# Kernel optimization log

Measured on AMD Instinct MI355X. Metric: run time of the kernel, lower is better.

Reference implementation:

```python
import jax, jax.numpy as jnp
import numpy as np
from jax import lax

B, C, H, W = 32, 512, 14, 14
NA = 9
N = H * W * NA  # 1764 anchors per image
IOU_THR = 0.3
SCORE_THR = 0.5
TOPK = 50


def setup_inputs() -> dict:
    key = jax.random.key(0)
    ks = jax.random.split(key, 8)
    def w(k, shape):
        return jax.random.normal(k, shape, jnp.float32) * 0.01  # nn.init.normal_(std=0.01)
    inp = {"features": jax.random.normal(ks[0], (B, C, H, W), jnp.float32)}
    # bbox head: 512->256 (GN32) ->128 (GN16) ->128 (GN16) -> 4*NA (1x1)
    inp["b1w"] = w(ks[1], (256, 512, 3, 3)); inp["b1b"] = jnp.zeros(256)
    inp["bg1w"] = jnp.ones(256); inp["bg1b"] = jnp.zeros(256)
    inp["b2w"] = w(ks[2], (128, 256, 3, 3)); inp["b2b"] = jnp.zeros(128)
    inp["bg2w"] = jnp.ones(128); inp["bg2b"] = jnp.zeros(128)
    inp["b3w"] = w(ks[3], (128, 128, 3, 3)); inp["b3b"] = jnp.zeros(128)
    inp["bg3w"] = jnp.ones(128); inp["bg3b"] = jnp.zeros(128)
    inp["b4w"] = w(ks[4], (4 * NA, 128, 1, 1)); inp["b4b"] = jnp.zeros(4 * NA)
    # classification head: 512->256 (GN32) ->128 (GN16) -> NA (1x1)
    inp["c1w"] = w(ks[5], (256, 512, 3, 3)); inp["c1b"] = jnp.zeros(256)
    inp["cg1w"] = jnp.ones(256); inp["cg1b"] = jnp.zeros(256)
    inp["c2w"] = w(ks[6], (128, 256, 3, 3)); inp["c2b"] = jnp.zeros(128)
    inp["cg2w"] = jnp.ones(128); inp["cg2b"] = jnp.zeros(128)
    inp["c3w"] = w(ks[7], (NA, 128, 1, 1)); inp["c3b"] = jnp.zeros(NA)
    return inp


def conv(x, w, b):
    k = w.shape[-1]
    pad = ((k // 2, k // 2), (k // 2, k // 2))
    y = lax.conv_general_dilated(x, w, (1, 1), pad, dimension_numbers=("NCHW", "OIHW", "NCHW"))
    return y + b[None, :, None, None]


def group_norm(x, w, b, groups, eps=1e-5):
    Bn, Cn, Hn, Wn = x.shape
    xg = x.reshape(Bn, groups, Cn // groups, Hn, Wn)
    mu = xg.mean(axis=(2, 3, 4), keepdims=True)
    var = xg.var(axis=(2, 3, 4), keepdims=True)
    xg = (xg - mu) * lax.rsqrt(var + eps)
    return xg.reshape(Bn, Cn, Hn, Wn) * w[None, :, None, None] + b[None, :, None, None]


def gelu(x):
    return jax.nn.gelu(x, approximate=False)  # torch nn.GELU default (erf)


def nms_single(boxes, scores):
    # boxes [N,4], scores [N]; greedy NMS, fixed-shape padded output [TOPK,5]
    valid = scores > SCORE_THR
    boxes = jnp.clip(boxes, 0.0, 1.0)
    order = jnp.argsort(-jnp.where(valid, scores, -jnp.inf))  # desc, invalid last
    b = boxes[order]; s = scores[order]; v = valid[order]
    x1 = jnp.maximum(b[:, None, 0], b[None, :, 0])
    y1 = jnp.maximum(b[:, None, 1], b[None, :, 1])
    x2 = jnp.minimum(b[:, None, 2], b[None, :, 2])
    y2 = jnp.minimum(b[:, None, 3], b[None, :, 3])
    inter = jnp.clip(x2 - x1, 0.0) * jnp.clip(y2 - y1, 0.0)
    area = (b[:, 2] - b[:, 0]) * (b[:, 3] - b[:, 1])
    iou = inter / (area[:, None] + area[None, :] - inter)
    # torch keeps when iou < thr; NaN compares False -> suppressed. Replicate exactly:
    suppress = jnp.logical_not(iou < IOU_THR)  # [N,N] bool
    idxs = jnp.arange(N)
    def body(suppressed, xs):
        row, i, vi = xs
        keep_i = vi & jnp.logical_not(suppressed[i])
        return suppressed | (keep_i & row & (idxs > i)), keep_i
    _, keep = lax.scan(body, jnp.zeros(N, bool), (suppress, idxs, v))
    kept_scores = jnp.where(keep, s, -1.0)
    topv, topi = lax.top_k(kept_scores, TOPK)  # first <=50 kept in score order
    out_boxes = jnp.where(topv[:, None] > 0.0, b[topi], 0.0)
    return jnp.concatenate([out_boxes, topv[:, None]], axis=-1)  # [TOPK, 5]; score=-1 marks pad


def _forward(features, b1w, b1b, bg1w, bg1b, b2w, b2b, bg2w, bg2b, b3w, b3b, bg3w, bg3b, b4w, b4b, c1w, c1b, cg1w, cg1b, c2w, c2b, cg2w, cg2b, c3w, c3b):
    bs = features.shape[0]
    h = group_norm(gelu(conv(features, b1w, b1b)), bg1w, bg1b, 32)
    h = group_norm(gelu(conv(h, b2w, b2b)), bg2w, bg2b, 16)
    h = group_norm(gelu(conv(h, b3w, b3b)), bg3w, bg3b, 16)
    bbox = conv(h, b4w, b4b).transpose(0, 2, 3, 1).reshape(bs, -1, 4)  # [B,N,4]
    h = group_norm(gelu(conv(features, c1w, c1b)), cg1w, cg1b, 32)
    h = group_norm(gelu(conv(h, c2w, c2b)), cg2w, cg2b, 16)
    conf = jax.nn.sigmoid(conv(h, c3w, c3b).transpose(0, 2, 3, 1).reshape(bs, -1))  # [B,N]
    return jax.vmap(nms_single)(bbox, conf)  # [B,TOPK,5]


def reference(features, b1w, b1b, bg1w, bg1b, b2w, b2b, bg2w, bg2b, b3w, b3b, bg3w, bg3b, b4w, b4b, c1w, c1b, cg1w, cg1b, c2w, c2b, cg2w, cg2b, c3w, c3b):
    return _forward(features, b1w, b1b, bg1w, bg1b, b2w, b2b, bg2w, bg2b, b3w, b3b, bg3w, bg3b, b4w, b4b, c1w, c1b, cg1w, cg1b, c2w, c2b, cg2w, cg2b, c3w, c3b)
```

## Files before the change

kernel.cpp:

```cpp
#include <hip/hip_runtime.h>
#include <hip/hip_bf16.h>
#include <math.h>

#define CHUNK 16
#define NN 1764
#define SORTN 2048

typedef float v2f __attribute__((ext_vector_type(2)));

template<int Co, int Ci>
__device__ inline void seg_pack_pk(const float* __restrict__ src, float* __restrict__ dst, int i) {
  int co = i / (Ci * 9); int rem = i - co * (Ci * 9); int ci = rem / 9; int k = rem - ci * 9;
  int p = (co >> 5) * 16 + (co & 15);
  int h = (co & 31) >> 4;
  dst[((size_t)ci * (Co >> 1) + p) * 20 + 2 * k + h] = src[i];
}
template<int Co, int CiK>
__device__ inline void seg_tr(const float* __restrict__ src, float* __restrict__ dst, int i) {
  int co = i / CiK; int cik = i - co * CiK;
  dst[cik * Co + co] = src[i];
}

__device__ inline void seg_wino_u(const float* __restrict__ src, float* __restrict__ dst, int i) {
  int ci = i >> 8;
  int co = i & 255;
  const float* g = src + ((size_t)co * 512 + ci) * 9;
  float g00=g[0],g01=g[1],g02=g[2],g10=g[3],g11=g[4],g12=g[5],g20=g[6],g21=g[7],g22=g[8];
  float a[4][3];
  a[0][0]=g00; a[0][1]=g01; a[0][2]=g02;
  a[1][0]=0.5f*(g00+g10+g20); a[1][1]=0.5f*(g01+g11+g21); a[1][2]=0.5f*(g02+g12+g22);
  a[2][0]=0.5f*(g00-g10+g20); a[2][1]=0.5f*(g01-g11+g21); a[2][2]=0.5f*(g02-g12+g22);
  a[3][0]=g20; a[3][1]=g21; a[3][2]=g22;
  const int p = (co >> 5) * 16 + (co & 15);
  const int h = (co & 31) >> 4;
#pragma unroll
  for (int r4 = 0; r4 < 4; ++r4) {
    float u0 = a[r4][0];
    float u1 = 0.5f * (a[r4][0] + a[r4][1] + a[r4][2]);
    float u2 = 0.5f * (a[r4][0] - a[r4][1] + a[r4][2]);
    float u3 = a[r4][2];
    float uv[4] = {u0, u1, u2, u3};
#pragma unroll
    for (int c4 = 0; c4 < 4; ++c4) {
      int pos = r4 * 4 + c4;
      dst[(((size_t)pos * 512 + ci) * 128 + p) * 2 + h] = uv[c4];
    }
  }
}

__global__ void wtrans_all(
  const float* __restrict__ b1w, const float* __restrict__ c1w,
  const float* __restrict__ b2w, const float* __restrict__ c2w,
  const float* __restrict__ b3w, const float* __restrict__ b4w,
  const float* __restrict__ c3w,
  float* __restrict__ ub, float* __restrict__ uc,
  float* __restrict__ wp2b, float* __restrict__ wp2c,
  float* __restrict__ wp3b, float* __restrict__ wt4b, float* __restrict__ wt3c)
{
  int j = blockIdx.x * blockDim.x + threadIdx.x;
  if (j < 131072) { seg_wino_u(b1w, ub, j); return; } j -= 131072;
  if (j < 131072) { seg_wino_u(c1w, uc, j); return; } j -= 131072;
  if (j < 294912) { seg_pack_pk<128, 256>(b2w, wp2b, j); return; } j -= 294912;
  if (j < 294912) { seg_pack_pk<128, 256>(c2w, wp2c, j); return; } j -= 294912;
  if (j < 147456) { seg_pack_pk<128, 128>(b3w, wp3b, j); return; } j -= 147456;
  if (j < 4608)   { seg_tr<36, 128>(b4w, wt4b, j); return; }  j -= 4608;
  if (j < 1152)   { seg_tr<9, 128>(c3w, wt3c, j); return; }
}

__global__ __launch_bounds__(256) void wino_in(
    const float* __restrict__ f, float* __restrict__ V)
{
  const int b = blockIdx.x, cig = blockIdx.y, tid = threadIdx.x;
  if (tid >= 196) return;
  const int ci = cig * 4 + tid / 49;
  const int t  = tid % 49;
  const int ty = t / 7, tx = t % 7;
  const float* fp = f + ((size_t)b * 512 + ci) * 196;
  const int y0 = 2 * ty - 1, x0 = 2 * tx - 1;
  float d[4][4];
#pragma unroll
  for (int i = 0; i < 4; ++i) {
    const int y = y0 + i;
#pragma unroll
    for (int j = 0; j < 4; ++j) {
      const int x = x0 + j;
      d[i][j] = (y >= 0 && y < 14 && x >= 0 && x < 14) ? fp[y * 14 + x] : 0.0f;
    }
  }
  float tr[4][4];
#pragma unroll
  for (int j = 0; j < 4; ++j) {
    tr[0][j] = d[0][j] - d[2][j];
    tr[1][j] = d[1][j] + d[2][j];
    tr[2][j] = d[2][j] - d[1][j];
    tr[3][j] = d[1][j] - d[3][j];
  }
  const size_t m = (size_t)b * 49 + t;
#pragma unroll
  for (int i = 0; i < 4; ++i) {
    float v0 = tr[i][0] - tr[i][2];
    float v1 = tr[i][1] + tr[i][2];
    float v2 = tr[i][2] - tr[i][1];
    float v3 = tr[i][1] - tr[i][3];
    V[((size_t)(i * 4 + 0) * 512 + ci) * 1568 + m] = v0;
    V[((size_t)(i * 4 + 1) * 512 + ci) * 1568 + m] = v1;
    V[((size_t)(i * 4 + 2) * 512 + ci) * 1568 + m] = v2;
    V[((size_t)(i * 4 + 3) * 512 + ci) * 1568 + m] = v3;
  }
}

__global__ __launch_bounds__(256, 2) void wino_gemm(
    const float* __restrict__ V, const float* __restrict__ U, float* __restrict__ M)
{
  const int pos = blockIdx.x;
  const int mb  = blockIdx.y;
  const int q   = blockIdx.z;
  const int head = q >> 1;
  const int pb   = q & 1;
  const int tid = threadIdx.x;
  const int col = tid & 15;
  const int r   = tid >> 4;

  __shared__ float vbuf[2][16][64];
  __shared__ float ubuf[2][16][128];

  const float* Uh = U + (size_t)head * 2097152;
  float* Mh = M + (size_t)head * 6422528;
  const int m0 = mb * 64;

  const int sci  = tid >> 4;
  const int voff = (tid & 15) * 4;
  const int uoff = (tid & 15) * 8;
  const float* vsrc = V + ((size_t)pos * 512 + sci) * 1568 + m0 + voff;
  const float* usrc = Uh + ((size_t)pos * 512 + sci) * 256 + pb * 128 + uoff;

  {
    float4 a0 = *(const float4*)(vsrc);
    float4 b0 = *(const float4*)(usrc);
    float4 b1 = *(const float4*)(usrc + 4);
    *(float4*)&vbuf[0][sci][voff] = a0;
    *(float4*)&ubuf[0][sci][uoff] = b0; *(float4*)&ubuf[0][sci][uoff + 4] = b1;
  }
  __syncthreads();

  v2f acc[4][4];
#pragma unroll
  for (int g = 0; g < 4; ++g)
#pragma unroll
    for (int j = 0; j < 4; ++j) acc[g][j] = (v2f)(0.0f);

  int cur = 0;
  for (int cb = 0; cb < 32; ++cb) {
    const bool more = (cb + 1 < 32);
    float4 a0, b0, b1;
    if (more) {
      const float* vs = vsrc + (size_t)(cb + 1) * 16 * 1568;
      const float* us = usrc + (size_t)(cb + 1) * 16 * 256;
      a0 = *(const float4*)vs;
      b0 = *(const float4*)us; b1 = *(const float4*)(us + 4);
    }
#pragma unroll
    for (int ci = 0; ci < 16; ++ci) {
      v2f u2[4];
#pragma unroll
      for (int g = 0; g < 4; ++g)
        u2[g] = *(const v2f*)&ubuf[cur][ci][(g * 16 + col) * 2];
      const float4* vp = (const float4*)&vbuf[cur][ci][r * 4];
      float4 v0 = vp[0];
      float vv[4] = {v0.x, v0.y, v0.z, v0.w};
#pragma unroll
      for (int j = 0; j < 4; ++j) {
        v2f s2 = (v2f){vv[j], vv[j]};
#pragma unroll
        for (int g = 0; g < 4; ++g)
          acc[g][j] = __builtin_elementwise_fma(u2[g], s2, acc[g][j]);
      }
    }
    if (more) {
      *(float4*)&vbuf[cur ^ 1][sci][voff] = a0;
      *(float4*)&ubuf[cur ^ 1][sci][uoff] = b0; *(float4*)&ubuf[cur ^ 1][sci][uoff + 4] = b1;
    }
    __syncthreads();
    cur ^= 1;
  }

  const int mm = m0 + r * 4;
  if (mm < 1568) {
#pragma unroll
    for (int g = 0; g < 4; ++g) {
      const int p = pb * 64 + g * 16 + col;
      const int cox = (p >> 4) * 32 + (p & 15);
      float* ox = Mh + ((size_t)pos * 256 + cox) * 1568 + mm;
      float* oy = ox + (size_t)16 * 1568;
#pragma unroll
      for (int j = 0; j < 4; ++j) { ox[j] = acc[g][j].x; oy[j] = acc[g][j].y; }
    }
  }
}

__global__ __launch_bounds__(256) void wino_out_gn(
    const float* __restrict__ M,
    const float* __restrict__ bsb, const float* __restrict__ bsc,
    const float* __restrict__ gwb, const float* __restrict__ gwc,
    const float* __restrict__ gbb, const float* __restrict__ gbc,
    float* __restrict__ outb, float* __restrict__ outc)
{
  const int bx = blockIdx.x;
  const int b  = blockIdx.y;
  const int head = bx >> 4, cog = bx & 15;
  const int tid = threadIdx.x;
  const float* Mh = M + (size_t)head * 6422528;
  const float* bs = head ? bsc : bsb;
  const float* gw = head ? gwc : gwb;
  const float* gb = head ? gbc : gbb;
  float* out      = head ? outc : outb;
  const int co0 = cog * 16;

  __shared__ float red[4][4];
  __shared__ float stats[4];

  const bool pa = tid < 196;
  const int csub = tid / 49;
  const int t    = tid % 49;
  const int ty = t / 7, tx = t % 7;
  const size_t mt = (size_t)b * 49 + t;

  float y4[4][4];
  float s = 0.f, q = 0.f;
  if (pa) {
#pragma unroll
    for (int cc = 0; cc < 4; ++cc) {
      const int co = co0 + csub * 4 + cc;
      const float* mp = Mh + (size_t)co * 1568 + mt;
      float m16[16];
#pragma unroll
      for (int pos = 0; pos < 16; ++pos)
        m16[pos] = mp[(size_t)pos * 401408];
      float Z0[4], Z1[4];
#pragma unroll
      for (int j = 0; j < 4; ++j) {
        Z0[j] = m16[0 * 4 + j] + m16[1 * 4 + j] + m16[2 * 4 + j];
        Z1[j] = m16[1 * 4 + j] - m16[2 * 4 + j] - m16[3 * 4 + j];
      }
      const float bias = bs[co];
      float yv[4];
      yv[0] = Z0[0] + Z0[1] + Z0[2];
      yv[1] = Z0[1] - Z0[2] - Z0[3];
      yv[2] = Z1[0] + Z1[1] + Z1[2];
      yv[3] = Z1[1] - Z1[2] - Z1[3];
#pragma unroll
      for (int k = 0; k < 4; ++k) {
        float x = yv[k] + bias;
        float g = 0.5f * x * (1.0f + erff(x * 0.70710678118654752440f));
        y4[cc][k] = g;
        s += g; q += g * g;
      }
    }
  }
  float s0 = (pa && csub < 2) ? s : 0.f, q0 = (pa && csub < 2) ? q : 0.f;
  float s1 = (pa && csub >= 2) ? s : 0.f, q1 = (pa && csub >= 2) ? q : 0.f;
#pragma unroll
  for (int off = 32; off > 0; off >>= 1) {
    s0 += __shfl_down(s0, off, 64); q0 += __shfl_down(q0, off, 64);
    s1 += __shfl_down(s1, off, 64); q1 += __shfl_down(q1, off, 64);
  }
  const int wave = tid >> 6, lane = tid & 63;
  if (lane == 0) { red[wave][0] = s0; red[wave][1] = q0; red[wave][2] = s1; red[wave][3] = q1; }
  __syncthreads();
  if (tid == 0) {
    float S0 = red[0][0] + red[1][0] + red[2][0] + red[3][0];
    float Q0 = red[0][1] + red[1][1] + red[2][1] + red[3][1];
    float S1 = red[0][2] + red[1][2] + red[2][2] + red[3][2];
    float Q1 = red[0][3] + red[1][3] + red[2][3] + red[3][3];
    float m0 = S0 * (1.0f / 1568.0f);
    float v0 = Q0 * (1.0f / 1568.0f) - m0 * m0;
    float m1 = S1 * (1.0f / 1568.0f);
    float v1 = Q1 * (1.0f / 1568.0f) - m1 * m1;
    stats[0] = m0; stats[1] = 1.0f / sqrtf(v0 + 1e-5f);
    stats[2] = m1; stats[3] = 1.0f / sqrtf(v1 + 1e-5f);
  }
  __syncthreads();
  if (pa) {
    const float mg = (csub < 2) ? stats[0] : stats[2];
    const float iv = (csub < 2) ? stats[1] : stats[3];
#pragma unroll
    for (int cc = 0; cc < 4; ++cc) {
      const int co = co0 + csub * 4 + cc;
      const float w = gw[co], bb2 = gb[co];
      float* op = out + ((size_t)b * 256 + co) * 196;
#pragma unroll
      for (int dy = 0; dy < 2; ++dy)
#pragma unroll
        for (int dx = 0; dx < 2; ++dx) {
          float yv = (y4[cc][dy * 2 + dx] - mg) * iv * w + bb2;
          op[(2 * ty + dy) * 14 + (2 * tx + dx)] = yv;
        }
    }
  }
}

template<int COPT>
__global__ __launch_bounds__(256, 2) void conv3x3_part(
    const float* __restrict__ in0, const float* __restrict__ in1,
    const float* __restrict__ wt0, const float* __restrict__ wt1,
    float* __restrict__ po0, float* __restrict__ po1,
    int Cin, int Cout, int cobPerHead, int cinPerSplit, size_t sStride)
{
  constexpr int NP = COPT / 2;
  constexpr int NPP = 16 * NP;
  constexpr int NPAIR = 8 * NPP;
  const int tid = threadIdx.x;
  const int bx  = blockIdx.x;
  const int b   = blockIdx.y;
  const int s   = blockIdx.z;
  const int head = bx / cobPerHead;
  const int cob  = bx - head * cobPerHead;
  const float* in  = head ? in1  : in0;
  const float* wt  = head ? wt1  : wt0;
  float* po        = head ? po1  : po0;
  const int co0 = cob * (16 * COPT);

  const int col = tid & 15;
  const int r   = tid >> 4;
  const bool ract = r < 14;

  __shared__ float tile[2][CHUNK][16][16];
  __shared__ float wbuf[2][8][NPP][20];

  {
    float* tz = &tile[0][0][0][0];
    for (int i = tid; i < 2 * CHUNK * 256; i += 256) tz[i] = 0.0f;
  }
  __syncthreads();

  const int p = tid;
  const bool pa = p < 196;
  const int prow = p / 14, pcol = p - prow * 14;
  const float* inb = in + (size_t)b * Cin * 196;
  const int cb0 = (s * cinPerSplit) / CHUNK;
  const int nch = cinPerSplit / CHUNK;
  const int CoutH = Cout >> 1;

  const int sciL = tid / NPP;
  const int spp  = tid - sciL * NPP;
  const bool sact = tid < NPAIR;
  const int spidx = ((co0 >> 5) + (spp >> 4)) * 16 + (spp & 15);

  if (pa) {
#pragma unroll
    for (int ci = 0; ci < CHUNK; ++ci)
      tile[0][ci][prow + 1][pcol + 1] = inb[(cb0 * CHUNK + ci) * 196 + p];
  }
  if (sact) {
    const float4* src = (const float4*)(wt + ((size_t)(cb0 * CHUNK + sciL) * CoutH + spidx) * 20);
    float4 q0 = src[0], q1 = src[1], q2 = src[2], q3 = src[3], q4 = src[4];
    float4* dst = (float4*)&wbuf[0][sciL][spp][0];
    dst[0] = q0; dst[1] = q1; dst[2] = q2; dst[3] = q3; dst[4] = q4;
  }
  __syncthreads();

  v2f acc[NP][14];
#pragma unroll
  for (int g = 0; g < NP; ++g)
#pragma unroll
    for (int j = 0; j < 14; ++j) acc[g][j] = (v2f)(0.0f);

  int wcur = 0;
  for (int lcb = 0; lcb < nch; ++lcb) {
    const int cbg = cb0 + lcb;
    const int cur = lcb & 1;
    const bool more = (lcb + 1 < nch);
    float v[CHUNK];
    if (more && pa) {
#pragma unroll
      for (int ci = 0; ci < CHUNK; ++ci)
        v[ci] = inb[((cbg + 1) * CHUNK + ci) * 196 + p];
    }
#pragma unroll
    for (int half = 0; half < 2; ++half) {
      const bool hasNext = (half == 0) || more;
      const int nbase = (half == 0) ? (cbg * CHUNK + 8) : ((cbg + 1) * CHUNK);
      float4 q0, q1, q2, q3, q4;
      if (hasNext && sact) {
        const float4* src = (const float4*)(wt + ((size_t)(nbase + sciL) * CoutH + spidx) * 20);
        q0 = src[0]; q1 = src[1]; q2 = src[2]; q3 = src[3]; q4 = src[4];
      }
      if (ract) {
#pragma unroll
        for (int ciL = 0; ciL < 8; ++ciL) {
          const int ci = half * 8 + ciL;
          v2f w2[NP][9];
#pragma unroll
          for (int g = 0; g < NP; ++g) {
            const float4* wq = (const float4*)&wbuf[wcur][ciL][g * 16 + col][0];
            float4 a0 = wq[0], a1 = wq[1], a2 = wq[2], a3 = wq[3], a4 = wq[4];
            w2[g][0] = (v2f){a0.x, a0.y}; w2[g][1] = (v2f){a0.z, a0.w};
            w2[g][2] = (v2f){a1.x, a1.y}; w2[g][3] = (v2f){a1.z, a1.w};
            w2[g][4] = (v2f){a2.x, a2.y}; w2[g][5] = (v2f){a2.z, a2.w};
            w2[g][6] = (v2f){a3.x, a3.y}; w2[g][7] = (v2f){a3.z, a3.w};
            w2[g][8] = (v2f){a4.x, a4.y};
          }
          float nb[3][16];
#pragma unroll
          for (int dr = 0; dr < 3; ++dr) {
            const float4* rp = (const float4*)(&tile[cur][ci][r + dr][0]);
            float4 a = rp[0], bq = rp[1], cq = rp[2], dq = rp[3];
            nb[dr][0]  = a.x;  nb[dr][1]  = a.y;  nb[dr][2]  = a.z;  nb[dr][3]  = a.w;
            nb[dr][4]  = bq.x; nb[dr][5]  = bq.y; nb[dr][6]  = bq.z; nb[dr][7]  = bq.w;
            nb[dr][8]  = cq.x; nb[dr][9]  = cq.y; nb[dr][10] = cq.z; nb[dr][11] = cq.w;
            nb[dr][12] = dq.x; nb[dr][13] = dq.y; nb[dr][14] = dq.z; nb[dr][15] = dq.w;
          }
#pragma unroll
          for (int ky = 0; ky < 3; ++ky)
#pragma unroll
            for (int kx = 0; kx < 3; ++kx) {
#pragma unroll
              for (int g = 0; g < NP; ++g) {
                v2f w = w2[g][ky * 3 + kx];
#pragma unroll
                for (int j = 0; j < 14; ++j) {
                  float s_ = nb[ky][j + kx];
                  v2f nbv = (v2f){s_, s_};
                  acc[g][j] = __builtin_elementwise_fma(w, nbv, acc[g][j]);
                }
              }
            }
        }
      }
      if (hasNext && sact) {
        float4* dst = (float4*)&wbuf[wcur ^ 1][sciL][spp][0];
        dst[0] = q0; dst[1] = q1; dst[2] = q2; dst[3] = q3; dst[4] = q4;
      }
      if (half == 1 && more && pa) {
#pragma unroll
        for (int ci = 0; ci < CHUNK; ++ci)
          tile[1 - cur][ci][prow + 1][pcol + 1] = v[ci];
      }
      __syncthreads();
      wcur ^= 1;
    }
  }

  if (ract) {
#pragma unroll
    for (int g = 0; g < NP; ++g) {
      const int ocx = 32 * g + col;
      const int ocy = ocx + 16;
      float* opx = po + (size_t)s * sStride + ((size_t)b * Cout + co0 + ocx) * 196 + r * 14;
      float* opy = po + (size_t)s * sStride + ((size_t)b * Cout + co0 + ocy) * 196 + r * 14;
#pragma unroll
      for (int j = 0; j < 14; ++j) { opx[j] = acc[g][j].x; opy[j] = acc[g][j].y; }
    }
  }
}

template<int S>
__global__ __launch_bounds__(256) void combine_gn(
    const float* __restrict__ po0, const float* __restrict__ po1,
    const float* __restrict__ bs0, const float* __restrict__ bs1,
    const float* __restrict__ gw0, const float* __restrict__ gw1,
    const float* __restrict__ gb0, const float* __restrict__ gb1,
    float* __restrict__ out0, float* __restrict__ out1,
    int Cout, int cobPerHead, size_t sStride)
{
  const int tid = threadIdx.x, bx = blockIdx.x, b = blockIdx.y;
  const int head = bx / cobPerHead, cob = bx - head * cobPerHead;
  const float* po = head ? po1 : po0;
  const float* bs = head ? bs1 : bs0;
  const float* gw = head ? gw1 : gw0;
  const float* gb = head ? gb1 : gb0;
  float* out      = head ? out1 : out0;
  const int co0 = cob * 16;

  __shared__ float red[4][4];
  __shared__ float stats[4];

  const int p = tid;
  const bool pa = p < 196;
  float v[16];
  float s0 = 0.f, q0 = 0.f, s1 = 0.f, q1 = 0.f;
  if (pa) {
#pragma unroll
    for (int c = 0; c < 16; ++c) {
      const size_t base = ((size_t)b * Cout + co0 + c) * 196 + p;
      float x = bs[co0 + c];
#pragma unroll
      for (int s = 0; s < S; ++s) x += po[base + (size_t)s * sStride];
      float g = 0.5f * x * (1.0f + erff(x * 0.70710678118654752440f));
      v[c] = g;
      if (c < 8) { s0 += g; q0 += g * g; } else { s1 += g; q1 += g * g; }
    }
  }
#pragma unroll
  for (int off = 32; off > 0; off >>= 1) {
    s0 += __shfl_down(s0, off, 64); q0 += __shfl_down(q0, off, 64);
    s1 += __shfl_down(s1, off, 64); q1 += __shfl_down(q1, off, 64);
  }
  const int wave = tid >> 6, lane = tid & 63;
  if (lane == 0) { red[wave][0] = s0; red[wave][1] = q0; red[wave][2] = s1; red[wave][3] = q1; }
  __syncthreads();
  if (tid == 0) {
    float S0 = red[0][0] + red[1][0] + red[2][0] + red[3][0];
    float Q0 = red[0][1] + red[1][1] + red[2][1] + red[3][1];
    float S1 = red[0][2] + red[1][2] + red[2][2] + red[3][2];
    float Q1 = red[0][3] + red[1][3] + red[2][3] + red[3][3];
    float m0 = S0 * (1.0f / 1568.0f);
    float v0 = Q0 * (1.0f / 1568.0f) - m0 * m0;
    float m1 = S1 * (1.0f / 1568.0f);
    float v1 = Q1 * (1.0f / 1568.0f) - m1 * m1;
    stats[0] = m0; stats[1] = 1.0f / sqrtf(v0 + 1e-5f);
    stats[2] = m1; stats[3] = 1.0f / sqrtf(v1 + 1e-5f);
  }
  __syncthreads();
  if (pa) {
    float m0 = stats[0], i0 = stats[1], m1 = stats[2], i1 = stats[3];
#pragma unroll
    for (int c = 0; c < 16; ++c) {
      float m  = (c < 8) ? m0 : m1;
      float iv = (c < 8) ? i0 : i1;
      float y = (v[c] - m) * iv * gw[co0 + c] + gb[co0 + c];
      out[((size_t)b * Cout + co0 + c) * 196 + p] = y;
    }
  }
}

__global__ __launch_bounds__(512) void nms_kernel(
  const float* __restrict__ tb, const float* __restrict__ tc,
  const float* __restrict__ wtb, const float* __restrict__ wtc,
  const float* __restrict__ bb,  const float* __restrict__ bc,
  float* __restrict__ bbox, float* __restrict__ out)
{
  const int b = blockIdx.x, tid = threadIdx.x;
  __shared__ unsigned long long key[SORTN];
  __shared__ float sx1[NN], sy1[NN], sx2[NN], sy2[NN], sar[NN], ssc[NN];
  __shared__ unsigned char sup[NN];
  __shared__ int sV, sMin;

  if (tid == 0) sV = 0;
  for (int i = NN + tid; i < SORTN; i += 512) key[i] = 0ull;

  int cntv = 0;
  if (tid < 196) {
    const int p = tid;
    float ab[36], ac[9];
#pragma unroll
    for (int o = 0; o < 36; ++o) ab[o] = bb[o];
#pragma unroll
    for (int o = 0; o < 9; ++o)  ac[o] = bc[o];
    const float* pb = tb + (size_t)b * 128 * 196 + p;
    const float* pc = tc + (size_t)b * 128 * 196 + p;
    for (int ci = 0; ci < 128; ++ci) {
      float xb = pb[ci * 196];
      float xc = pc[ci * 196];
      const float* wB = wtb + ci * 36;
      const float* wC = wtc + ci * 9;
#pragma unroll
      for (int o = 0; o < 36; ++o) ab[o] = fmaf(wB[o], xb, ab[o]);
#pragma unroll
      for (int o = 0; o < 9; ++o)  ac[o] = fmaf(wC[o], xc, ac[o]);
    }
    float* bp = bbox + ((size_t)b * NN) * 4 + (size_t)p * 36;
#pragma unroll
    for (int o = 0; o < 36; ++o) bp[o] = ab[o];
#pragma unroll
    for (int a = 0; a < 9; ++a) {
      float s = 1.0f / (1.0f + expf(-ac[a]));
      const int n = p * 9 + a;
      unsigned rank = (unsigned)(NN - 1 - n);
      unsigned long long k;
      if (s > 0.5f) { k = (((unsigned long long)__float_as_uint(s)) << 32) | rank; cntv++; }
      else k = (unsigned long long)rank;
      key[n] = k;
    }
  }
  atomicAdd(&sV, cntv);
  __syncthreads();
  const int V = sV;

  for (int kk = 2; kk <= SORTN; kk <<= 1) {
    for (int j = kk >> 1; j > 0; j >>= 1) {
      for (int i = tid; i < SORTN; i += 512) {
        int ixj = i ^ j;
        if (ixj > i) {
          unsigned long long a = key[i], c = key[ixj];
          bool dirDesc = ((i & kk) == 0);
          if ((a < c) == dirDesc) { key[i] = c; key[ixj] = a; }
        }
      }
      __syncthreads();
    }
  }

  const float* bbb = bbox + (size_t)b * NN * 4;
  for (int i = tid; i < V; i += 512) {
    unsigned long long k = key[i];
    int idx = NN - 1 - (int)(unsigned)(k & 0xFFFFFFFFull);
    float s = __uint_as_float((unsigned)(k >> 32));
    const float* bp = bbb + (size_t)idx * 4;
    float x1 = fminf(fmaxf(bp[0], 0.0f), 1.0f);
    float y1 = fminf(fmaxf(bp[1], 0.0f), 1.0f);
    float x2 = fminf(fmaxf(bp[2], 0.0f), 1.0f);
    float y2 = fminf(fmaxf(bp[3], 0.0f), 1.0f);
    sx1[i] = x1; sy1[i] = y1; sx2[i] = x2; sy2[i] = y2;
    sar[i] = (x2 - x1) * (y2 - y1);
    ssc[i] = s;
    sup[i] = 0;
  }
  __syncthreads();

  int kept = 0, cur = 0;
  float* ob = out + (size_t)b * 50 * 5;
  while (kept < 50 && cur < V) {
    int nxt = -1;
    for (int base = cur; base < V; base += 512) {
      if (tid == 0) sMin = 0x7FFFFFFF;
      __syncthreads();
      int i = base + tid;
      if (i < V && !sup[i]) atomicMin(&sMin, i);
      __syncthreads();
      if (sMin != 0x7FFFFFFF) { nxt = sMin; break; }
    }
    if (nxt < 0) break;
    float kx1 = sx1[nxt], ky1 = sy1[nxt], kx2 = sx2[nxt], ky2 = sy2[nxt], ka = sar[nxt];
    if (tid == 0) {
      float* rr = ob + kept * 5;
      rr[0] = kx1; rr[1] = ky1; rr[2] = kx2; rr[3] = ky2; rr[4] = ssc[nxt];
    }
    kept++;
    for (int jj = nxt + 1 + tid; jj < V; jj += 512) {
      if (!sup[jj]) {
        float xx1 = fmaxf(kx1, sx1[jj]);
        float yy1 = fmaxf(ky1, sy1[jj]);
        float xx2 = fminf(kx2, sx2[jj]);
        float yy2 = fminf(ky2, sy2[jj]);
        float inter = fmaxf(xx2 - xx1, 0.0f) * fmaxf(yy2 - yy1, 0.0f);
        float iou = inter / ((ka + sar[jj]) - inter);
        if (!(iou < 0.3f)) sup[jj] = 1;
      }
    }
    cur = nxt + 1;
    __syncthreads();
  }
  for (int rr = kept + tid; rr < 50; rr += 512) {
    float* qq = ob + rr * 5;
    qq[0] = 0.0f; qq[1] = 0.0f; qq[2] = 0.0f; qq[3] = 0.0f; qq[4] = -1.0f;
  }
}

extern "C" void kernel_launch(void* const* d_in, const int* in_sizes, int n_in,
                              void* d_out, int out_size, void* d_ws, size_t ws_size,
                              hipStream_t stream)
{
  const float* features = (const float*)d_in[0];
  const float* b1w = (const float*)d_in[1];  const float* b1b = (const float*)d_in[2];
  const float* bg1w = (const float*)d_in[3]; const float* bg1b = (const float*)d_in[4];
  const float* b2w = (const float*)d_in[5];  const float* b2b = (const float*)d_in[6];
  const float* bg2w = (const float*)d_in[7]; const float* bg2b = (const float*)d_in[8];
  const float* b3w = (const float*)d_in[9];  const float* b3b = (const float*)d_in[10];
  const float* bg3w = (const float*)d_in[11]; const float* bg3b = (const float*)d_in[12];
  const float* b4w = (const float*)d_in[13]; const float* b4b = (const float*)d_in[14];
  const float* c1w = (const float*)d_in[15]; const float* c1b = (const float*)d_in[16];
  const float* cg1w = (const float*)d_in[17]; const float* cg1b = (const float*)d_in[18];
  const float* c2w = (const float*)d_in[19]; const float* c2b = (const float*)d_in[20];
  const float* cg2w = (const float*)d_in[21]; const float* cg2b = (const float*)d_in[22];
  const float* c3w = (const float*)d_in[23]; const float* c3b = (const float*)d_in[24];

  float* ws = (float*)d_ws;
  float* U    = ws; ws += 4194304;
  float* wp2b = ws; ws += 327680;
  float* wp2c = ws; ws += 327680;
  float* wp3b = ws; ws += 163840;
  float* wt4b = ws; ws += 4608;
  float* wt3c = ws; ws += 1152;
  float* t1b  = ws; ws += 1605632;
  float* t1c  = ws; ws += 1605632;
  float* t2b  = ws; ws += 802816;
  float* t2c  = ws; ws += 802816;
  float* V    = ws; ws += 12845056;
  float* M    = ws; ws += 12845056;
  float* bbox = ws; ws += 225792;
  float* P    = V;
  float* t3b  = t1b;

  wtrans_all<<<3927, 256, 0, stream>>>(b1w, c1w, b2w, c2w, b3w, b4w, c3w,
                                       U, U + 2097152, wp2b, wp2c, wp3b, wt4b, wt3c);

  wino_in<<<dim3(32, 128), 256, 0, stream>>>(features, V);
  wino_gemm<<<dim3(16, 25, 4), 256, 0, stream>>>(V, U, M);
  wino_out_gn<<<dim3(32, 32), 256, 0, stream>>>(M, b1b, c1b, bg1w, cg1w, bg1b, cg1b, t1b, t1c);

  {
    const size_t sStr = (size_t)32 * 128 * 196;
    conv3x3_part<4><<<dim3(4, 32, 4), 256, 0, stream>>>(
        t1b, t1c, wp2b, wp2c, P, P + 4 * sStr, 256, 128, 2, 64, sStr);
    combine_gn<4><<<dim3(16, 32), 256, 0, stream>>>(
        P, P + 4 * sStr, b2b, c2b, bg2w, cg2w, bg2b, cg2b, t2b, t2c, 128, 8, sStr);
  }
  {
    const size_t sStr = (size_t)32 * 128 * 196;
    conv3x3_part<2><<<dim3(4, 32, 4), 256, 0, stream>>>(
        t2b, t2b, wp3b, wp3b, P, P, 128, 128, 4, 32, sStr);
    combine_gn<4><<<dim3(8, 32), 256, 0, stream>>>(
        P, P, b3b, b3b, bg3w, bg3w, bg3b, bg3b, t3b, t3b, 128, 8, sStr);
  }

  nms_kernel<<<32, 512, 0, stream>>>(t3b, t2c, wt4b, wt3c, b4b, c3b, bbox, (float*)d_out);
}
```

Baseline: 666.0 us.

## Load Winograd GEMM tiles directly into LDS and re-interleave U layout

The Winograd GEMM tile loads now use global_load_lds builtins, which write straight into the double-buffered shared memory instead of staging through registers. The transformed weights U are permuted at pack time so each thread reads its four column pairs with two float4 LDS reads instead of four v2f reads. This is meant to reduce register pressure, VGPR-to-LDS store instructions and LDS read count in the inner loop. It relies on the direct-to-LDS builtin's per-wave addressing being correct and on the weight layout matching the new read pattern.

```diff
diff --git a/kernel.cpp b/kernel.cpp
--- a/kernel.cpp
+++ b/kernel.cpp
@@ -7,6 +7,12 @@
 #define SORTN 2048
 
 typedef float v2f __attribute__((ext_vector_type(2)));
+
+__device__ inline void gl_lds16(const float* g, float* l) {
+  __builtin_amdgcn_global_load_lds(
+      (const __attribute__((address_space(1))) void*)g,
+      (__attribute__((address_space(3))) void*)l, 16, 0, 0);
+}
 
 template<int Co, int Ci>
 __device__ inline void seg_pack_pk(const float* __restrict__ src, float* __restrict__ dst, int i) {
@@ -31,8 +37,11 @@
   a[1][0]=0.5f*(g00+g10+g20); a[1][1]=0.5f*(g01+g11+g21); a[1][2]=0.5f*(g02+g12+g22);
   a[2][0]=0.5f*(g00-g10+g20); a[2][1]=0.5f*(g01-g11+g21); a[2][2]=0.5f*(g02-g12+g22);
   a[3][0]=g20; a[3][1]=g21; a[3][2]=g22;
-  const int p = (co >> 5) * 16 + (co & 15);
+  const int p_old = (co >> 5) * 16 + (co & 15);
   const int h = (co & 31) >> 4;
+  const int pb = p_old >> 6, loc = p_old & 63;
+  const int gg = loc >> 4, col = loc & 15;
+  const int P = pb * 64 + (gg >> 1) * 32 + col * 2 + (gg & 1);
 #pragma unroll
   for (int r4 = 0; r4 < 4; ++r4) {
     float u0 = a[r4][0];
@@ -43,7 +52,7 @@
 #pragma unroll
     for (int c4 = 0; c4 < 4; ++c4) {
       int pos = r4 * 4 + c4;
-      dst[(((size_t)pos * 512 + ci) * 128 + p) * 2 + h] = uv[c4];
+      dst[(((size_t)pos * 512 + ci) * 128 + P) * 2 + h] = uv[c4];
     }
   }
 }
@@ -120,6 +129,7 @@
   const int tid = threadIdx.x;
   const int col = tid & 15;
   const int r   = tid >> 4;
+  const int wv  = tid >> 6;
 
   __shared__ float vbuf[2][16][64];
   __shared__ float ubuf[2][16][128];
@@ -128,19 +138,16 @@
   float* Mh = M + (size_t)head * 6422528;
   const int m0 = mb * 64;
 
-  const int sci  = tid >> 4;
-  const int voff = (tid & 15) * 4;
-  const int uoff = (tid & 15) * 8;
-  const float* vsrc = V + ((size_t)pos * 512 + sci) * 1568 + m0 + voff;
-  const float* usrc = Uh + ((size_t)pos * 512 + sci) * 256 + pb * 128 + uoff;
-
-  {
-    float4 a0 = *(const float4*)(vsrc);
-    float4 b0 = *(const float4*)(usrc);
-    float4 b1 = *(const float4*)(usrc + 4);
-    *(float4*)&vbuf[0][sci][voff] = a0;
-    *(float4*)&ubuf[0][sci][uoff] = b0; *(float4*)&ubuf[0][sci][uoff + 4] = b1;
-  }
+  const float* vg  = V + ((size_t)pos * 512 + (tid >> 4)) * 1568 + m0 + (tid & 15) * 4;
+  const int c1 = 256 + tid;
+  const float* ug0 = Uh + ((size_t)pos * 512 + (tid >> 5)) * 256 + pb * 128 + (tid & 31) * 4;
+  const float* ug1 = Uh + ((size_t)pos * 512 + (c1 >> 5)) * 256 + pb * 128 + (c1 & 31) * 4;
+  float* vls = ((float*)vbuf) + wv * 256;
+  float* uls = ((float*)ubuf) + wv * 256;
+
+  gl_lds16(vg, vls);
+  gl_lds16(ug0, uls);
+  gl_lds16(ug1, uls + 1024);
   __syncthreads();
 
   v2f acc[4][4];
@@ -151,20 +158,19 @@
 
   int cur = 0;
   for (int cb = 0; cb < 32; ++cb) {
-    const bool more = (cb + 1 < 32);
-    float4 a0, b0, b1;
-    if (more) {
-      const float* vs = vsrc + (size_t)(cb + 1) * 16 * 1568;
-      const float* us = usrc + (size_t)(cb + 1) * 16 * 256;
-      a0 = *(const float4*)vs;
-      b0 = *(const float4*)us; b1 = *(const float4*)(us + 4);
+    if (cb + 1 < 32) {
+      const int nb = cur ^ 1;
+      gl_lds16(vg + (size_t)(cb + 1) * 16 * 1568, vls + nb * 1024);
+      gl_lds16(ug0 + (size_t)(cb + 1) * 16 * 256, uls + nb * 2048);
+      gl_lds16(ug1 + (size_t)(cb + 1) * 16 * 256, uls + nb * 2048 + 1024);
     }
 #pragma unroll
     for (int ci = 0; ci < 16; ++ci) {
-      v2f u2[4];
-#pragma unroll
-      for (int g = 0; g < 4; ++g)
-        u2[g] = *(const v2f*)&ubuf[cur][ci][(g * 16 + col) * 2];
+      const float4* uq0 = (const float4*)&ubuf[cur][ci][col * 4];
+      const float4* uq1 = (const float4*)&ubuf[cur][ci][64 + col * 4];
+      float4 a = uq0[0], bq = uq1[0];
+      v2f u2[4] = { (v2f){a.x, a.y}, (v2f){a.z, a.w},
+                    (v2f){bq.x, bq.y}, (v2f){bq.z, bq.w} };
       const float4* vp = (const float4*)&vbuf[cur][ci][r * 4];
       float4 v0 = vp[0];
       float vv[4] = {v0.x, v0.y, v0.z, v0.w};
@@ -175,10 +181,6 @@
         for (int g = 0; g < 4; ++g)
           acc[g][j] = __builtin_elementwise_fma(u2[g], s2, acc[g][j]);
       }
-    }
-    if (more) {
-      *(float4*)&vbuf[cur ^ 1][sci][voff] = a0;
-      *(float4*)&ubuf[cur ^ 1][sci][uoff] = b0; *(float4*)&ubuf[cur ^ 1][sci][uoff + 4] = b1;
     }
     __syncthreads();
     cur ^= 1;
```

Measured after the change: 670.5 us. No clear change (+0.7%).
